# Optimization experiments

Measured on AMD Instinct MI355X. Metric: run time of the kernel, lower is better.

## Reference

```python
import jax, jax.numpy as jnp
import numpy as np

DIMS = (8, 8, 16, 16)   # 4D lattice, prod = 16384 sites
ND = len(DIMS)
N_IN = 4
N_OUT = 4
NC = 3
KERNEL_SIZE = 2
DILATION = 0
INIT_W = 1.0

W_IN = 2 * N_IN + 1                                  # 9
T_W = 2 * (N_IN * (KERNEL_SIZE - 1) * ND) + 1        # 33


def cconj(w):
    # swap matrix indices (axes 3,4) and negate imaginary part (last axis)
    wT = jnp.swapaxes(w, 3, 4)
    return wT * jnp.array([1.0, -1.0], dtype=w.dtype)


def complex_einsum(pattern, a, b, conj_a=1, conj_b=1):
    aR, aI = a[..., 0], conj_a * a[..., 1]
    bR, bI = b[..., 0], conj_b * b[..., 1]
    cR = jnp.einsum(pattern, aR, bR) - jnp.einsum(pattern, aI, bI)
    cI = jnp.einsum(pattern, aR, bI) + jnp.einsum(pattern, aI, bR)
    return jnp.stack((cR, cI), axis=-1)


def shift(a, axis, orientation):
    # dim 1 is flattened lattice; unflatten, roll along lattice axis, re-flatten
    o_s = a.shape
    n_s = (o_s[0],) + DIMS + o_s[2:]
    return jnp.roll(a.reshape(n_s), orientation, axis=axis + 1).reshape(o_s)


def transport(u, w, axis):
    # positive-orientation gauge transport: U w(x+mu) U^dagger
    ws = shift(w, axis, -1)
    ua = u[:, :, axis]                                 # [b, x, nc, nc, 2]
    wt = complex_einsum('bxij,bxwjk->bxwik', ua, ws)
    wt = complex_einsum('bxwij,bxkj->bxwik', wt, ua, conj_b=-1)
    return wt


def setup_inputs() -> dict:
    key = jax.random.key(0)
    k1, k2 = jax.random.split(key)
    n_sites = int(np.prod(DIMS))
    x = jax.random.normal(k1, (1, n_sites, ND + N_IN, NC, NC, 2), dtype=jnp.float32)
    std = INIT_W * np.sqrt(1.0 / (W_IN * T_W))
    weight = jax.random.normal(k2, (N_OUT, W_IN, T_W), dtype=jnp.float32) * std
    return {"x": x, "weight": weight}


def reference(x, weight):
    u, w = x[:, :, :ND], x[:, :, ND:]
    transported = []
    for axis in range(ND):
        wt = w
        for d in range(1, KERNEL_SIZE):
            for _ in range(DILATION + 1):
                wt = transport(u, wt, axis)
            transported.append(wt)
    t_w = jnp.concatenate(transported, axis=2)          # [b, x, n_in*(K-1)*ND, nc, nc, 2]

    w_full = jnp.concatenate([w, cconj(w)], axis=2)
    t_w_full = jnp.concatenate([t_w, cconj(t_w)], axis=2)

    # unit element channel
    unit = jnp.stack((jnp.eye(NC, dtype=x.dtype), jnp.zeros((NC, NC), dtype=x.dtype)), axis=-1)
    b, n_sites = x.shape[0], x.shape[1]
    unit_t = jnp.broadcast_to(unit[None, None, None], (b, n_sites, 1, NC, NC, 2))
    w_full = jnp.concatenate([w_full, unit_t], axis=2)       # [b, x, 9, nc, nc, 2]
    t_w_full = jnp.concatenate([t_w_full, unit_t], axis=2)   # [b, x, 33, nc, nc, 2]

    # bilinear gauge-covariant products, then weight contraction
    ww = complex_einsum('bxvij,bxwjk->bxvwik', w_full, t_w_full)  # [b, x, 9, 33, nc, nc, 2]
    w_out = jnp.einsum('uvw,bxvwijc->bxuijc', weight, ww)         # [b, x, n_out, nc, nc, 2]

    return jnp.concatenate([u, w_out], axis=2)
```

## Files before the change

kernel.cpp:

```cpp
#include <hip/hip_runtime.h>
#include <stdint.h>


typedef float v2f __attribute__((ext_vector_type(2)));

#define SPB 8
#define TPB 256
#define NSITES 16384
#define TS2_SITE 146
#define NWGT 1188

#if defined(__has_builtin)
#if __has_builtin(__builtin_elementwise_fma)
#define HAVE_EW_FMA 1
#endif
#endif

__device__ __forceinline__ v2f pkfma(v2f a, v2f b, v2f c){
#ifdef HAVE_EW_FMA
    return __builtin_elementwise_fma(a, b, c);
#else
    v2f r; r.x = fmaf(a.x, b.x, c.x); r.y = fmaf(a.y, b.y, c.y); return r;
#endif
}
__device__ __forceinline__ v2f spl(float s){ return (v2f){s, s}; }
__device__ __forceinline__ v2f pn (float s){ return (v2f){s, -s}; }
__device__ __forceinline__ v2f np (float s){ return (v2f){-s, s}; }
__device__ __forceinline__ v2f swp(v2f a){ return __builtin_shufflevector(a, a, 1, 0); }
__device__ __forceinline__ v2f zero2(){ return (v2f){0.f, 0.f}; }

__device__ __forceinline__ int neigh(int s, int a){
    if (a == 3) return (s & ~15)        | ((s + 1)    & 15);
    if (a == 2) return (s & ~(15 << 4)) | ((s + 16)   & (15 << 4));
    if (a == 1) return (s & ~(7 << 8))  | ((s + 256)  & (7 << 8));
    return              (s & ~(7 << 11))| ((s + 2048) & (7 << 11));
}

__global__ __launch_bounds__(TPB, 3)
void gcm_fused(const float* __restrict__ xp,
               const float* __restrict__ wgt,
               float* __restrict__ outp)
{
    __shared__ v2f lt[SPB * TS2_SITE];
    __shared__ float wsm[NWGT];
    const v2f* x2 = (const v2f*)xp;
    v2f* o2 = (v2f*)outp;

    const int tid = threadIdx.x;
    const int h   = tid & 7;
    const int u   = (tid >> 3) & 3;
    const int sl  = tid >> 5;
    const int s   = blockIdx.x * SPB + sl;
    const int g   = h & 3;

    #pragma unroll 1
    for (int idx = tid; idx < NWGT; idx += TPB) wsm[idx] = wgt[idx];

    if (h < 4){
        v2f uc[9], wc[9];
        {
            const v2f* up = x2 + (s * 8 + u) * 9;
            #pragma unroll
            for (int e = 0; e < 9; e++) uc[e] = up[e];
        }
        const int sn = neigh(s, u);
        {
            const v2f* wp = x2 + (sn * 8 + 4 + h) * 9;
            #pragma unroll
            for (int e = 0; e < 9; e++) wc[e] = wp[e];
        }
        v2f t1[9];
        #pragma unroll
        for (int r = 0; r < 3; r++){
            #pragma unroll
            for (int k = 0; k < 3; k++){
                v2f acc = zero2();
                #pragma unroll
                for (int j = 0; j < 3; j++){
                    v2f a_ = uc[r*3+j], b_ = wc[j*3+k];
                    acc = pkfma(spl(a_.x), b_, acc);
                    acc = pkfma(np(a_.y), swp(b_), acc);
                }
                t1[r*3+k] = acc;
            }
        }
        v2f* dst = &lt[sl * TS2_SITE + (u * 4 + h) * 9];
        #pragma unroll
        for (int r = 0; r < 3; r++){
            #pragma unroll
            for (int k = 0; k < 3; k++){
                v2f acc = zero2();
                #pragma unroll
                for (int j = 0; j < 3; j++){
                    v2f a_ = t1[r*3+j], b_ = uc[k*3+j];
                    acc = pkfma(pn(a_.x), b_, acc);
                    acc = pkfma(spl(a_.y), swp(b_), acc);
                }
                dst[r*3+k] = acc;
            }
        }
    } else if (h == 4){
        const v2f* src = x2 + (s * 8 + u) * 9;
        v2f* dst = o2 + (s * 8 + u) * 9;
        #pragma unroll
        for (int e = 0; e < 9; e++) dst[e] = src[e];
    }
    __syncthreads();

    v2f M[9], cc[9];
    #pragma unroll
    for (int e = 0; e < 9; e++){ M[e] = zero2(); cc[e] = zero2(); }

    const float* wu  = wsm + u * 297;
    const float* wvh = wu + h * 33;
    const float* wu8 = wu + 8 * 33;

    const v2f* tbase = &lt[sl * TS2_SITE];

    #pragma unroll 1
    for (int w16 = 0; w16 < 16; w16++){
        const v2f* tp = tbase + w16 * 9;
        v2f tc[9];
        #pragma unroll
        for (int e = 0; e < 9; e++) tc[e] = tp[e];
        float a = wvh[w16], b = wvh[16 + w16];
        #pragma unroll
        for (int i = 0; i < 3; i++){
            #pragma unroll
            for (int j = 0; j < 3; j++){
                const int e = i*3+j, eT = j*3+i;
                M[e] = pkfma(spl(a), tc[e],  M[e]);
                M[e] = pkfma(pn(b),  tc[eT], M[e]);
            }
        }
    }

    #pragma unroll
    for (int q = 0; q < 2; q++){
        const int w16 = 2 * h + q;
        const v2f* tp = tbase + w16 * 9;
        v2f tc[9];
        #pragma unroll
        for (int e = 0; e < 9; e++) tc[e] = tp[e];
        float c8 = wu8[w16], d8 = wu8[16 + w16];
        #pragma unroll
        for (int i = 0; i < 3; i++){
            #pragma unroll
            for (int j = 0; j < 3; j++){
                const int e = i*3+j, eT = j*3+i;
                cc[e] = pkfma(spl(c8), tc[e],  cc[e]);
                cc[e] = pkfma(pn(d8),  tc[eT], cc[e]);
            }
        }
    }

    {
        float ch = wvh[32];
        M[0].x += ch; M[4].x += ch; M[8].x += ch;
        if (h == 0){
            float e8 = wu8[32];
            cc[0].x += e8; cc[4].x += e8; cc[8].x += e8;
        }
    }

    v2f A[9];
    {
        const v2f* wp = x2 + (s * 8 + 4 + g) * 9;
        v2f wgr[9];
        #pragma unroll
        for (int e = 0; e < 9; e++) wgr[e] = wp[e];
        const bool dag = (h >= 4);
        #pragma unroll
        for (int i = 0; i < 3; i++){
            #pragma unroll
            for (int j = 0; j < 3; j++){
                v2f p = wgr[i*3+j];
                v2f q = wgr[j*3+i]; q.y = -q.y;
                A[i*3+j] = dag ? q : p;
            }
        }
    }

    #pragma unroll
    for (int i = 0; i < 3; i++){
        #pragma unroll
        for (int k = 0; k < 3; k++){
            v2f acc = cc[i*3+k];
            #pragma unroll
            for (int j = 0; j < 3; j++){
                v2f a_ = A[i*3+j];
                v2f m  = M[j*3+k];
                acc = pkfma(spl(a_.x), m,      acc);
                acc = pkfma(np(a_.y),  swp(m), acc);
            }
            cc[i*3+k] = acc;
        }
    }

    #pragma unroll
    for (int e = 0; e < 9; e++){
        #pragma unroll
        for (int d = 1; d <= 4; d <<= 1){
            cc[e].x += __shfl_xor(cc[e].x, d);
            cc[e].y += __shfl_xor(cc[e].y, d);
        }
    }
    if (h == 0){
        v2f* dst = o2 + (s * 8 + 4 + u) * 9;
        #pragma unroll
        for (int e = 0; e < 9; e++) dst[e] = cc[e];
    }
}

extern "C" void kernel_launch(void* const* d_in, const int* in_sizes, int n_in,
                              void* d_out, int out_size, void* d_ws, size_t ws_size,
                              hipStream_t stream)
{
    const float* x = (const float*)d_in[0];
    const float* w = (const float*)d_in[1];
    float* out = (float*)d_out;
    dim3 grid(NSITES / SPB);
    dim3 block(TPB);
    hipLaunchKernelGGL(gcm_fused, grid, block, 0, stream, x, w, out);
}
```

Before: 83.54 us.

## Remap threads to four per (site,out) and double-buffer transported tile loads

Changes the thread mapping from eight threads per (site, output) pair to four, so every thread does transport work and no lanes sit idle. Each thread now accumulates two M matrices, one for w and one for its dagger, and folds the extra unit-channel contribution into the main loop. Shared-memory tiles are double-buffered so the next tile loads while the current one is being computed. Sites per block double, the shuffle reduction shrinks to two steps, and occupancy drops to two blocks per CU, with higher register pressure in exchange.

```diff
diff --git a/kernel.cpp b/kernel.cpp
--- a/kernel.cpp
+++ b/kernel.cpp
@@ -4,7 +4,7 @@
 
 typedef float v2f __attribute__((ext_vector_type(2)));
 
-#define SPB 8
+#define SPB 16
 #define TPB 256
 #define NSITES 16384
 #define TS2_SITE 146
@@ -36,7 +36,9 @@
     return              (s & ~(7 << 11))| ((s + 2048) & (7 << 11));
 }
 
-__global__ __launch_bounds__(TPB, 3)
+struct Coefs { float a1, b1, a2, b2, c8, d8; };
+
+__global__ __launch_bounds__(TPB, 2)
 void gcm_fused(const float* __restrict__ xp,
                const float* __restrict__ wgt,
                float* __restrict__ outp)
@@ -47,16 +49,15 @@
     v2f* o2 = (v2f*)outp;
 
     const int tid = threadIdx.x;
-    const int h   = tid & 7;
-    const int u   = (tid >> 3) & 3;
-    const int sl  = tid >> 5;
+    const int g   = tid & 3;
+    const int u   = (tid >> 2) & 3;
+    const int sl  = tid >> 4;
     const int s   = blockIdx.x * SPB + sl;
-    const int g   = h & 3;
 
     #pragma unroll 1
     for (int idx = tid; idx < NWGT; idx += TPB) wsm[idx] = wgt[idx];
 
-    if (h < 4){
+    {
         v2f uc[9], wc[9];
         {
             const v2f* up = x2 + (s * 8 + u) * 9;
@@ -65,7 +66,7 @@
         }
         const int sn = neigh(s, u);
         {
-            const v2f* wp = x2 + (sn * 8 + 4 + h) * 9;
+            const v2f* wp = x2 + (sn * 8 + 4 + g) * 9;
             #pragma unroll
             for (int e = 0; e < 9; e++) wc[e] = wp[e];
         }
@@ -84,7 +85,7 @@
                 t1[r*3+k] = acc;
             }
         }
-        v2f* dst = &lt[sl * TS2_SITE + (u * 4 + h) * 9];
+        v2f* dst = &lt[sl * TS2_SITE + (u * 4 + g) * 9];
         #pragma unroll
         for (int r = 0; r < 3; r++){
             #pragma unroll
@@ -99,88 +100,88 @@
                 dst[r*3+k] = acc;
             }
         }
-    } else if (h == 4){
+    }
+    __syncthreads();
+
+    if (g == 1){
         const v2f* src = x2 + (s * 8 + u) * 9;
         v2f* dst = o2 + (s * 8 + u) * 9;
         #pragma unroll
         for (int e = 0; e < 9; e++) dst[e] = src[e];
     }
-    __syncthreads();
-
-    v2f M[9], cc[9];
-    #pragma unroll
-    for (int e = 0; e < 9; e++){ M[e] = zero2(); cc[e] = zero2(); }
+
+    v2f wg[9];
+    {
+        const v2f* wp = x2 + (s * 8 + 4 + g) * 9;
+        #pragma unroll
+        for (int e = 0; e < 9; e++) wg[e] = wp[e];
+    }
+
+    v2f M1[9], M2[9], cc[9];
+    #pragma unroll
+    for (int e = 0; e < 9; e++){
+        M1[e] = zero2(); M2[e] = zero2(); cc[e] = zero2();
+    }
 
     const float* wu  = wsm + u * 297;
-    const float* wvh = wu + h * 33;
+    const float* wuA = wu + g * 33;
+    const float* wuB = wu + (4 + g) * 33;
     const float* wu8 = wu + 8 * 33;
 
     const v2f* tbase = &lt[sl * TS2_SITE];
 
+    v2f tA[9], tB[9];
+    #pragma unroll
+    for (int e = 0; e < 9; e++) tA[e] = tbase[e];
+
+#define LOAD_TILE(dst, w)  { const v2f* _tp = tbase + (w) * 9; \
+    _Pragma("unroll") for (int e = 0; e < 9; e++) dst[e] = _tp[e]; }
+
+#define GET_COEF(C, w)  { C.a1 = wuA[w]; C.b1 = wuA[16 + (w)]; \
+    C.a2 = wuB[w]; C.b2 = wuB[16 + (w)]; \
+    const bool _m = (((w) >> 2) == g); \
+    C.c8 = _m ? wu8[w] : 0.f; C.d8 = _m ? wu8[16 + (w)] : 0.f; }
+
+#define COMPUTE(T, C) { _Pragma("unroll") for (int i = 0; i < 3; i++){ \
+        _Pragma("unroll") for (int j = 0; j < 3; j++){ \
+            const int e = i*3+j, eT = j*3+i; \
+            M1[e] = pkfma(spl(C.a1), T[e],  M1[e]); \
+            M1[e] = pkfma(pn(C.b1),  T[eT], M1[e]); \
+            M2[e] = pkfma(spl(C.a2), T[e],  M2[e]); \
+            M2[e] = pkfma(pn(C.b2),  T[eT], M2[e]); \
+            cc[e] = pkfma(spl(C.c8), T[e],  cc[e]); \
+            cc[e] = pkfma(pn(C.d8),  T[eT], cc[e]); } } }
+
     #pragma unroll 1
-    for (int w16 = 0; w16 < 16; w16++){
-        const v2f* tp = tbase + w16 * 9;
-        v2f tc[9];
-        #pragma unroll
-        for (int e = 0; e < 9; e++) tc[e] = tp[e];
-        float a = wvh[w16], b = wvh[16 + w16];
-        #pragma unroll
-        for (int i = 0; i < 3; i++){
-            #pragma unroll
-            for (int j = 0; j < 3; j++){
-                const int e = i*3+j, eT = j*3+i;
-                M[e] = pkfma(spl(a), tc[e],  M[e]);
-                M[e] = pkfma(pn(b),  tc[eT], M[e]);
-            }
-        }
-    }
-
-    #pragma unroll
-    for (int q = 0; q < 2; q++){
-        const int w16 = 2 * h + q;
-        const v2f* tp = tbase + w16 * 9;
-        v2f tc[9];
-        #pragma unroll
-        for (int e = 0; e < 9; e++) tc[e] = tp[e];
-        float c8 = wu8[w16], d8 = wu8[16 + w16];
-        #pragma unroll
-        for (int i = 0; i < 3; i++){
-            #pragma unroll
-            for (int j = 0; j < 3; j++){
-                const int e = i*3+j, eT = j*3+i;
-                cc[e] = pkfma(spl(c8), tc[e],  cc[e]);
-                cc[e] = pkfma(pn(d8),  tc[eT], cc[e]);
-            }
-        }
-    }
-
-    {
-        float ch = wvh[32];
-        M[0].x += ch; M[4].x += ch; M[8].x += ch;
-        if (h == 0){
+    for (int w16 = 0; w16 < 14; w16 += 2){
+        Coefs cA; GET_COEF(cA, w16);
+        LOAD_TILE(tB, w16 + 1);
+        COMPUTE(tA, cA);
+        Coefs cB; GET_COEF(cB, w16 + 1);
+        LOAD_TILE(tA, w16 + 2);
+        COMPUTE(tB, cB);
+    }
+    {
+        Coefs cA; GET_COEF(cA, 14);
+        LOAD_TILE(tB, 15);
+        COMPUTE(tA, cA);
+        Coefs cB; GET_COEF(cB, 15);
+        COMPUTE(tB, cB);
+    }
+#undef LOAD_TILE
+#undef GET_COEF
+#undef COMPUTE
+
+    {
+        float c1 = wuA[32], c2 = wuB[32];
+        M1[0].x += c1; M1[4].x += c1; M1[8].x += c1;
+        M2[0].x += c2; M2[4].x += c2; M2[8].x += c2;
+        if (g == 0){
             float e8 = wu8[32];
             cc[0].x += e8; cc[4].x += e8; cc[8].x += e8;
         }
     }
 
-    v2f A[9];
-    {
-        const v2f* wp = x2 + (s * 8 + 4 + g) * 9;
-        v2f wgr[9];
-        #pragma unroll
-        for (int e = 0; e < 9; e++) wgr[e] = wp[e];
-        const bool dag = (h >= 4);
-        #pragma unroll
-        for (int i = 0; i < 3; i++){
-            #pragma unroll
-            for (int j = 0; j < 3; j++){
-                v2f p = wgr[i*3+j];
-                v2f q = wgr[j*3+i]; q.y = -q.y;
-                A[i*3+j] = dag ? q : p;
-            }
-        }
-    }
-
     #pragma unroll
     for (int i = 0; i < 3; i++){
         #pragma unroll
@@ -188,24 +189,30 @@
             v2f acc = cc[i*3+k];
             #pragma unroll
             for (int j = 0; j < 3; j++){
-                v2f a_ = A[i*3+j];
-                v2f m  = M[j*3+k];
+                v2f a_ = wg[i*3+j];
+                v2f m  = M1[j*3+k];
                 acc = pkfma(spl(a_.x), m,      acc);
                 acc = pkfma(np(a_.y),  swp(m), acc);
             }
+            #pragma unroll
+            for (int j = 0; j < 3; j++){
+                v2f b_ = wg[j*3+i];
+                v2f m  = M2[j*3+k];
+                acc = pkfma(spl(b_.x), m,      acc);
+                acc = pkfma(pn(b_.y),  swp(m), acc);
+            }
             cc[i*3+k] = acc;
         }
     }
 
     #pragma unroll
     for (int e = 0; e < 9; e++){
-        #pragma unroll
-        for (int d = 1; d <= 4; d <<= 1){
-            cc[e].x += __shfl_xor(cc[e].x, d);
-            cc[e].y += __shfl_xor(cc[e].y, d);
-        }
-    }
-    if (h == 0){
+        cc[e].x += __shfl_xor(cc[e].x, 1);
+        cc[e].x += __shfl_xor(cc[e].x, 2);
+        cc[e].y += __shfl_xor(cc[e].y, 1);
+        cc[e].y += __shfl_xor(cc[e].y, 2);
+    }
+    if (g == 0){
         v2f* dst = o2 + (s * 8 + 4 + u) * 9;
         #pragma unroll
         for (int e = 0; e < 9; e++) dst[e] = cc[e];
```

Result: faster. 76.72 us (-8.2%).
